# Performance work log

Measured on AMD Instinct MI355X. Metric: run time of the kernel, lower is better.

The kernel has to match this reference:

```python
import jax, jax.numpy as jnp
import numpy as np
from jax import lax

B, N, C = 8, 1024, 768
H, D = 12, 64
K = 3  # conv kernel size


def dwconv_over_batch(x, w, b):
    """Faithful port of SpatialDepthWisePerHeadConvolution as used in this module.
    x: [B, N, H, D]. The original code treats dim0 (B) as the conv length axis.
    w: [H*D, 1, K] depthwise kernel, b: [H*D].
    Returns [B, N, H, D].
    """
    b_, n_, h_, d_ = x.shape
    xc = jnp.transpose(x, (1, 2, 3, 0)).reshape(n_, h_ * d_, b_)  # [N, HD, B]
    y = lax.conv_general_dilated(
        xc, w, window_strides=(1,), padding=[(K - 1, K - 1)],
        feature_group_count=h_ * d_, dimension_numbers=("NCH", "OIH", "NCH"))
    y = y[:, :, :b_] + b[None, :, None]  # causal slice (drop last K-1)
    return jnp.transpose(y.reshape(n_, h_, d_, b_), (3, 0, 1, 2))


def setup_inputs() -> dict:
    key = jax.random.key(0)
    ks = jax.random.split(key, 12)
    s = 0.02
    inp = {
        "x": jax.random.normal(ks[0], (B, N, C), jnp.float32),
        "wq": jax.random.normal(ks[1], (C, H * D), jnp.float32) * s,
        "wk": jax.random.normal(ks[2], (C, H * D), jnp.float32) * s,
        "wv": jax.random.normal(ks[3], (C, H * D), jnp.float32) * s,
        "bv": jnp.zeros((H * D,), jnp.float32),
        "cq_w": jax.random.normal(ks[4], (H * D, 1, K), jnp.float32) * s,
        "cq_b": jnp.zeros((H * D,), jnp.float32),
        "ck_w": jax.random.normal(ks[5], (H * D, 1, K), jnp.float32) * s,
        "ck_b": jnp.zeros((H * D,), jnp.float32),
        "cv_w": jax.random.normal(ks[6], (H * D, 1, K), jnp.float32) * s,
        "cv_b": jnp.zeros((H * D,), jnp.float32),
        "wo": jax.random.normal(ks[7], (C, C), jnp.float32) * s,
        "bo": jnp.zeros((C,), jnp.float32),
    }
    return inp


def reference(x, wq, wk, wv, bv, cq_w, cq_b, ck_w, ck_b, cv_w, cv_b, wo, bo):
    scale = (C // H) ** -0.5
    # linear -> [B,N,H,D]
    q = (x @ wq).reshape(B, N, H, D)
    k = (x @ wk).reshape(B, N, H, D)
    v = ((x @ wv) + bv).reshape(B, N, H, D)
    # per-head depthwise causal conv (over batch axis, as in the original code)
    q = dwconv_over_batch(q, cq_w, cq_b)
    k = dwconv_over_batch(k, ck_w, ck_b)
    v = dwconv_over_batch(v, cv_w, cv_b)
    # [B,H,N,D]
    q = jnp.transpose(q, (0, 2, 1, 3))
    k = jnp.transpose(k, (0, 2, 1, 3))
    v = jnp.transpose(v, (0, 2, 1, 3))
    scores = jnp.einsum("bhnd,bhmd->bhnm", q, k) * scale
    attn = jax.nn.softmax(scores, axis=-1)
    out = jnp.einsum("bhnm,bhmd->bhnd", attn, v)
    out = jnp.transpose(out, (0, 2, 1, 3)).reshape(B, N, C)
    return out @ wo + bo
```

## Files before the change

### kernel.cpp

```cpp
#include <hip/hip_runtime.h>
#include <math.h>

static constexpr int B_ = 8, N_ = 1024, C_ = 768, H_ = 12, D_ = 64;

typedef __bf16 bf16_t;
typedef bf16_t bf16x8 __attribute__((ext_vector_type(8)));
typedef float f32x4 __attribute__((ext_vector_type(4)));

#define MFMA32(a, b, c) __builtin_amdgcn_mfma_f32_16x16x32_bf16((a), (b), (c), 0, 0, 0)

__device__ __forceinline__ unsigned short f2bf(float f) {
    unsigned u = __builtin_bit_cast(unsigned, f);
    u += 0x7FFFu + ((u >> 16) & 1u);
    return (unsigned short)(u >> 16);
}

__device__ __forceinline__ float bf2f(unsigned short u) {
    return __builtin_bit_cast(float, (unsigned)u << 16);
}

__device__ __forceinline__ void gload16(void* lds, const void* g) {
    __builtin_amdgcn_global_load_lds(
        (const __attribute__((address_space(1))) unsigned int*)g,
        (__attribute__((address_space(3))) unsigned int*)lds, 16, 0, 0);
}

__device__ __forceinline__ int swz(int row, int kslot) {
    return row * 128 + (((kslot ^ row) & 7) << 4);
}

__global__ __launch_bounds__(256)
void castx_kernel(const float* __restrict__ in, unsigned short* __restrict__ out)
{
    const int i = blockIdx.x * 256 + threadIdx.x;
    const float4 a = ((const float4*)in)[2 * i];
    const float4 b = ((const float4*)in)[2 * i + 1];
    uint4 o;
    o.x = f2bf(a.x) | ((unsigned)f2bf(a.y) << 16);
    o.y = f2bf(a.z) | ((unsigned)f2bf(a.w) << 16);
    o.z = f2bf(b.x) | ((unsigned)f2bf(b.y) << 16);
    o.w = f2bf(b.z) | ((unsigned)f2bf(b.w) << 16);
    ((uint4*)out)[i] = o;
}

__global__ __launch_bounds__(256)
void castwT4_kernel(const float* w0, const float* w1, const float* w2, const float* w3,
                    unsigned short* o0, unsigned short* o1,
                    unsigned short* o2, unsigned short* o3)
{
    const float* w; unsigned short* wT;
    switch (blockIdx.z) {
        case 0:  w = w0; wT = o0; break;
        case 1:  w = w1; wT = o1; break;
        case 2:  w = w2; wT = o2; break;
        default: w = w3; wT = o3; break;
    }
    __shared__ float T[64][65];
    const int t = threadIdx.x;
    const int k0 = blockIdx.x * 64, n0 = blockIdx.y * 64;
    const int r = t >> 2, c0 = (t & 3) * 16;
#pragma unroll
    for (int j4 = 0; j4 < 4; ++j4) {
        const float4 v = *(const float4*)(w + (size_t)(k0 + r) * 768 + n0 + c0 + j4 * 4);
        T[r][c0 + j4 * 4 + 0] = v.x; T[r][c0 + j4 * 4 + 1] = v.y;
        T[r][c0 + j4 * 4 + 2] = v.z; T[r][c0 + j4 * 4 + 3] = v.w;
    }
    __syncthreads();
    const int nn = t >> 2;
    unsigned short o[16];
#pragma unroll
    for (int j = 0; j < 16; ++j) o[j] = f2bf(T[c0 + j][nn]);
    uint4* dst = (uint4*)(wT + (size_t)(n0 + nn) * 768 + k0 + c0);
    dst[0] = *(uint4*)(o); dst[1] = *(uint4*)(o + 8);
}

template <typename OutT>
__device__ __forceinline__ void gemm_body(const unsigned short* __restrict__ A,
                                          const unsigned short* __restrict__ BT,
                                          const float* __restrict__ bias,
                                          OutT* __restrict__ Cmat,
                                          int Ncols, int Kdim, int row0, int col0)
{
    __shared__ char As[128 * 128];
    __shared__ char Bs[128 * 128];

    const int tid = threadIdx.x, lane = tid & 63, w = tid >> 6;
    const int wr = w >> 1, wc = w & 1;
    const int slot = lane & 7, rsub = lane >> 3;

    f32x4 acc[4][4] = {};

    for (int k0 = 0; k0 < Kdim; k0 += 64) {
#pragma unroll
        for (int c = 0; c < 4; ++c) {
            const int chunk = c * 4 + w;
            const int r = chunk * 8 + rsub;
            gload16(As + chunk * 1024, A + (size_t)(row0 + r) * Kdim + k0 + 8 * (slot ^ (r & 7)));
            gload16(Bs + chunk * 1024, BT + (size_t)(col0 + r) * Kdim + k0 + 8 * (slot ^ (r & 7)));
        }
        __syncthreads();

#pragma unroll
        for (int kk = 0; kk < 2; ++kk) {
            const int kslot = kk * 4 + (lane >> 4);
            bf16x8 af[4], bf[4];
#pragma unroll
            for (int mi = 0; mi < 4; ++mi)
                af[mi] = *(const bf16x8*)(As + swz(wr * 64 + mi * 16 + (lane & 15), kslot));
#pragma unroll
            for (int ni = 0; ni < 4; ++ni)
                bf[ni] = *(const bf16x8*)(Bs + swz(wc * 64 + ni * 16 + (lane & 15), kslot));
#pragma unroll
            for (int mi = 0; mi < 4; ++mi)
#pragma unroll
                for (int ni = 0; ni < 4; ++ni)
                    acc[mi][ni] = MFMA32(af[mi], bf[ni], acc[mi][ni]);
        }
        __syncthreads();
    }

#pragma unroll
    for (int mi = 0; mi < 4; ++mi) {
        const int row = row0 + wr * 64 + mi * 16 + ((lane >> 4) << 2);
#pragma unroll
        for (int ni = 0; ni < 4; ++ni) {
            const int col = col0 + wc * 64 + ni * 16 + (lane & 15);
            const float bv_ = bias ? bias[col] : 0.f;
#pragma unroll
            for (int r = 0; r < 4; ++r) {
                const float v = acc[mi][ni][r] + bv_;
                if constexpr (sizeof(OutT) == 2)
                    Cmat[(size_t)(row + r) * Ncols + col] = (OutT)f2bf(v);
                else
                    Cmat[(size_t)(row + r) * Ncols + col] = v;
            }
        }
    }
}

__global__ __launch_bounds__(256)
void gemm_qkv(const unsigned short* __restrict__ xb,
              const unsigned short* __restrict__ wqT, const unsigned short* __restrict__ wkT,
              const unsigned short* __restrict__ wvT, const float* __restrict__ bv,
              unsigned short* __restrict__ q_lin, unsigned short* __restrict__ k_lin,
              unsigned short* __restrict__ v_lin)
{
    const int by = blockIdx.y, sel = by / 6, colt = by % 6;
    const unsigned short* BT; unsigned short* dst; const float* bias = nullptr;
    if (sel == 0)      { BT = wqT; dst = q_lin; }
    else if (sel == 1) { BT = wkT; dst = k_lin; }
    else               { BT = wvT; dst = v_lin; bias = bv; }
    gemm_body<unsigned short>(xb, BT, bias, dst, C_, C_, blockIdx.x * 128, colt * 128);
}

__global__ __launch_bounds__(256)
void gemm_proj(const unsigned short* __restrict__ A, const unsigned short* __restrict__ BT,
               const float* __restrict__ bias, float* __restrict__ Cmat)
{
    gemm_body<float>(A, BT, bias, Cmat, C_, C_, blockIdx.x * 128, blockIdx.y * 128);
}

__global__ __launch_bounds__(256)
void dwconv_qk(const unsigned short* __restrict__ qlin, const unsigned short* __restrict__ klin,
               const float* __restrict__ cq_w, const float* __restrict__ cq_b,
               const float* __restrict__ ck_w, const float* __restrict__ ck_b,
               unsigned short* __restrict__ qc, unsigned short* __restrict__ kc)
{
    const unsigned short* lin; const float* w; const float* bias;
    unsigned short* out;
    if (blockIdx.y == 0) { lin = qlin; w = cq_w; bias = cq_b; out = qc; }
    else                 { lin = klin; w = ck_w; bias = ck_b; out = kc; }

    const int i = blockIdx.x * 256 + threadIdx.x;
    const int c8 = i % (C_ / 8);
    const int n  = (i / (C_ / 8)) % N_;
    const int b  = i / ((C_ / 8) * N_);
    const int c  = c8 * 8;

    const uint4 z4 = make_uint4(0, 0, 0, 0);
    const uint4 x0 = (b >= 2) ? *(const uint4*)(lin + ((size_t)(b - 2) * N_ + n) * C_ + c) : z4;
    const uint4 x1 = (b >= 1) ? *(const uint4*)(lin + ((size_t)(b - 1) * N_ + n) * C_ + c) : z4;
    const uint4 x2 = *(const uint4*)(lin + ((size_t)b * N_ + n) * C_ + c);
    const unsigned short* u0 = (const unsigned short*)&x0;
    const unsigned short* u1 = (const unsigned short*)&x1;
    const unsigned short* u2 = (const unsigned short*)&x2;

    unsigned short y[8];
#pragma unroll
    for (int j = 0; j < 8; ++j) {
        const float v = w[(c + j) * 3 + 0] * bf2f(u0[j]) +
                        w[(c + j) * 3 + 1] * bf2f(u1[j]) +
                        w[(c + j) * 3 + 2] * bf2f(u2[j]) + bias[c + j];
        y[j] = f2bf(v);
    }
    const int h = c8 >> 3, d0 = (c8 & 7) * 8;
    *(uint4*)(out + (((size_t)b * H_ + h) * N_ + n) * 64 + d0) = *(uint4*)y;
}

__global__ __launch_bounds__(256)
void conv_v_transpose(const unsigned short* __restrict__ vlin, const float* __restrict__ w,
                      const float* __restrict__ bias, unsigned short* __restrict__ vt)
{
    __shared__ unsigned short T[64][72];
    const int t = threadIdx.x;
    const int n0 = blockIdx.x * 64, bh = blockIdx.y;
    const int b = bh / H_, h = bh % H_;
    const int r = t >> 2, c0 = (t & 3) * 16;
    const int cbase = h * 64 + c0;

    float acc[16];
#pragma unroll
    for (int i = 0; i < 16; ++i) acc[i] = bias[cbase + i];
#pragma unroll
    for (int j = 0; j < 3; ++j) {
        const int bb = b - 2 + j;
        if (bb < 0) continue;
        const unsigned short* src = vlin + ((size_t)bb * N_ + n0 + r) * C_ + cbase;
        const uint4 va = *(const uint4*)src;
        const uint4 vb2 = *(const uint4*)(src + 8);
        const unsigned short* u = (const unsigned short*)&va;
        const unsigned short* u2 = (const unsigned short*)&vb2;
#pragma unroll
        for (int i = 0; i < 8; ++i)  acc[i]     += w[(cbase + i) * 3 + j] * bf2f(u[i]);
#pragma unroll
        for (int i = 0; i < 8; ++i)  acc[8 + i] += w[(cbase + 8 + i) * 3 + j] * bf2f(u2[i]);
    }
    unsigned short tmp[16];
#pragma unroll
    for (int i = 0; i < 16; ++i) tmp[i] = f2bf(acc[i]);
    *(uint4*)&T[r][c0] = *(uint4*)tmp;
    *(uint4*)&T[r][c0 + 8] = *(uint4*)(tmp + 8);
    __syncthreads();

    const int d = t >> 2;
    unsigned short o[16];
#pragma unroll
    for (int i = 0; i < 16; ++i) o[i] = T[c0 + i][d];
    uint4* dst = (uint4*)(vt + ((size_t)bh * 64 + d) * N_ + n0 + c0);
    dst[0] = *(uint4*)o; dst[1] = *(uint4*)(o + 8);
}

__global__ __launch_bounds__(256)
void attn_mfma(const unsigned short* __restrict__ Qg, const unsigned short* __restrict__ Kg,
               const unsigned short* __restrict__ Vtg, unsigned short* __restrict__ Og)
{
    __shared__ char Pb[16384];
    __shared__ char Kb[2][8192];
    __shared__ char Vb[2][8192];

    const int tid = threadIdx.x, lane = tid & 63, w = tid >> 6;
    const int slot = lane & 7, rsub = lane >> 3;

    const int id = blockIdx.x;
    const int bh = (id & 7) * 12 + ((id >> 3) % 12);
    const int q0 = (id / 96) * 128;
    const int b = bh / H_, h = bh % H_;

    const unsigned short* Qp = Qg + (size_t)bh * N_ * 64;
    const unsigned short* Kp = Kg + (size_t)bh * N_ * 64;
    const unsigned short* Vp = Vtg + (size_t)bh * 64 * N_;

#pragma unroll
    for (int c = 0; c < 4; ++c) {
        const int chunk = c * 4 + w;
        const int r = chunk * 8 + rsub;
        gload16(Pb + chunk * 1024, Qp + (size_t)(q0 + r) * 64 + 8 * (slot ^ (r & 7)));
    }
#pragma unroll
    for (int c = 0; c < 2; ++c) {
        const int chunk = c * 4 + w;
        const int r = chunk * 8 + rsub;
        gload16(Kb[0] + chunk * 1024, Kp + (size_t)r * 64 + 8 * (slot ^ (r & 7)));
        gload16(Vb[0] + chunk * 1024, Vp + (size_t)r * N_ + 8 * (slot ^ (r & 7)));
    }
    __syncthreads();

    bf16x8 qf[2][2];
#pragma unroll
    for (int mi = 0; mi < 2; ++mi)
#pragma unroll
        for (int kk = 0; kk < 2; ++kk)
            qf[mi][kk] = *(const bf16x8*)(Pb + swz(w * 32 + mi * 16 + (lane & 15), kk * 4 + (lane >> 4)));

    f32x4 o[2][4] = {};
    float mrow[2][4], lrow[2][4];
#pragma unroll
    for (int mi = 0; mi < 2; ++mi)
#pragma unroll
        for (int r = 0; r < 4; ++r) { mrow[mi][r] = -1e30f; lrow[mi][r] = 0.f; }

    int buf = 0;
    for (int kt = 0; kt < N_ / 64; ++kt) {
        if (kt < N_ / 64 - 1) {
            const int nb = buf ^ 1;
#pragma unroll
            for (int c = 0; c < 2; ++c) {
                const int chunk = c * 4 + w;
                const int r = chunk * 8 + rsub;
                gload16(Kb[nb] + chunk * 1024, Kp + (size_t)((kt + 1) * 64 + r) * 64 + 8 * (slot ^ (r & 7)));
                gload16(Vb[nb] + chunk * 1024, Vp + (size_t)r * N_ + (kt + 1) * 64 + 8 * (slot ^ (r & 7)));
            }
        }

        f32x4 s[2][4] = {};
#pragma unroll
        for (int kk = 0; kk < 2; ++kk) {
            const int kslot = kk * 4 + (lane >> 4);
            bf16x8 kf[4];
#pragma unroll
            for (int ni = 0; ni < 4; ++ni)
                kf[ni] = *(const bf16x8*)(Kb[buf] + swz(ni * 16 + (lane & 15), kslot));
#pragma unroll
            for (int mi = 0; mi < 2; ++mi)
#pragma unroll
                for (int ni = 0; ni < 4; ++ni)
                    s[mi][ni] = MFMA32(qf[mi][kk], kf[ni], s[mi][ni]);
        }

#pragma unroll
        for (int mi = 0; mi < 2; ++mi) {
            float pv[4][4];
#pragma unroll
            for (int r = 0; r < 4; ++r) {
                const float a0 = s[mi][0][r] * 0.125f, a1 = s[mi][1][r] * 0.125f;
                const float a2 = s[mi][2][r] * 0.125f, a3 = s[mi][3][r] * 0.125f;
                pv[r][0] = a0; pv[r][1] = a1; pv[r][2] = a2; pv[r][3] = a3;
                float m0 = fmaxf(fmaxf(a0, a1), fmaxf(a2, a3));
#pragma unroll
                for (int mk = 1; mk < 16; mk <<= 1) m0 = fmaxf(m0, __shfl_xor(m0, mk));
                const float mold = mrow[mi][r];
                const float mnew = fmaxf(mold, m0);
                const float f = __expf(mold - mnew);
                mrow[mi][r] = mnew;
                float ssum = 0.f;
#pragma unroll
                for (int ni = 0; ni < 4; ++ni) {
                    const float e = __expf(pv[r][ni] - mnew);
                    pv[r][ni] = e; ssum += e;
                }
#pragma unroll
                for (int mk = 1; mk < 16; mk <<= 1) ssum += __shfl_xor(ssum, mk);
                lrow[mi][r] = lrow[mi][r] * f + ssum;
#pragma unroll
                for (int nd = 0; nd < 4; ++nd) o[mi][nd][r] *= f;
            }
            const int prow_base = w * 32 + mi * 16 + ((lane >> 4) << 2);
#pragma unroll
            for (int r = 0; r < 4; ++r) {
                const int m = prow_base + r;
                const int rowoff = m * 128, sw = (m & 7) << 4;
#pragma unroll
                for (int ni = 0; ni < 4; ++ni) {
                    const int col = ni * 16 + (lane & 15);
                    *(unsigned short*)(Pb + rowoff + ((col * 2) ^ sw)) = f2bf(pv[r][ni]);
                }
            }
        }

#pragma unroll
        for (int kk = 0; kk < 2; ++kk) {
            const int kslot = kk * 4 + (lane >> 4);
            bf16x8 pa[2], vf[4];
#pragma unroll
            for (int mi = 0; mi < 2; ++mi)
                pa[mi] = *(const bf16x8*)(Pb + swz(w * 32 + mi * 16 + (lane & 15), kslot));
#pragma unroll
            for (int nd = 0; nd < 4; ++nd)
                vf[nd] = *(const bf16x8*)(Vb[buf] + swz(nd * 16 + (lane & 15), kslot));
#pragma unroll
            for (int mi = 0; mi < 2; ++mi)
#pragma unroll
                for (int nd = 0; nd < 4; ++nd)
                    o[mi][nd] = MFMA32(pa[mi], vf[nd], o[mi][nd]);
        }

        __syncthreads();
        buf ^= 1;
    }

#pragma unroll
    for (int mi = 0; mi < 2; ++mi)
#pragma unroll
        for (int r = 0; r < 4; ++r) {
            const float inv = 1.0f / lrow[mi][r];
            const int qrow = q0 + w * 32 + mi * 16 + ((lane >> 4) << 2) + r;
            unsigned short* orow = Og + ((size_t)b * N_ + qrow) * C_ + h * D_ + (lane & 15);
#pragma unroll
            for (int nd = 0; nd < 4; ++nd) orow[nd * 16] = f2bf(o[mi][nd][r] * inv);
        }
}

extern "C" void kernel_launch(void* const* d_in, const int* in_sizes, int n_in,
                              void* d_out, int out_size, void* d_ws, size_t ws_size,
                              hipStream_t stream)
{
    (void)in_sizes; (void)n_in; (void)out_size; (void)ws_size;
    const float* x    = (const float*)d_in[0];
    const float* wq   = (const float*)d_in[1];
    const float* wk   = (const float*)d_in[2];
    const float* wv   = (const float*)d_in[3];
    const float* bv   = (const float*)d_in[4];
    const float* cq_w = (const float*)d_in[5];
    const float* cq_b = (const float*)d_in[6];
    const float* ck_w = (const float*)d_in[7];
    const float* ck_b = (const float*)d_in[8];
    const float* cv_w = (const float*)d_in[9];
    const float* cv_b = (const float*)d_in[10];
    const float* wo   = (const float*)d_in[11];
    const float* bo   = (const float*)d_in[12];
    float* out = (float*)d_out;

    char* wsb = (char*)d_ws;
    const size_t T  = (size_t)B_ * N_ * C_;
    const size_t WB = (size_t)2 * 589824;
    unsigned short* xb  = (unsigned short*)wsb;
    unsigned short* wqT = (unsigned short*)(wsb + 2 * T);
    unsigned short* wkT = wqT + 589824;
    unsigned short* wvT = wkT + 589824;
    unsigned short* woT = wvT + 589824;
    char* p = wsb + 2 * T + 4 * WB;
    unsigned short* q_lin = (unsigned short*)p;          p += 2 * T;
    unsigned short* k_lin = (unsigned short*)p;          p += 2 * T;
    unsigned short* v_lin = (unsigned short*)p;          p += 2 * T;
    unsigned short* qc    = (unsigned short*)p;          p += 2 * T;
    unsigned short* kc    = (unsigned short*)p;          p += 2 * T;
    unsigned short* vt    = (unsigned short*)p;          p += 2 * T;
    unsigned short* attn_out = xb;

    const int M = B_ * N_;

    castx_kernel<<<dim3((int)(T / 8 / 256)), 256, 0, stream>>>(x, xb);
    castwT4_kernel<<<dim3(12, 12, 4), 256, 0, stream>>>(wq, wk, wv, wo, wqT, wkT, wvT, woT);

    gemm_qkv<<<dim3(M / 128, 18), 256, 0, stream>>>(xb, wqT, wkT, wvT, bv, q_lin, k_lin, v_lin);

    dwconv_qk<<<dim3((int)(T / 8 / 256), 2), 256, 0, stream>>>(
        q_lin, k_lin, cq_w, cq_b, ck_w, ck_b, qc, kc);
    conv_v_transpose<<<dim3(N_ / 64, B_ * H_), 256, 0, stream>>>(v_lin, cv_w, cv_b, vt);

    attn_mfma<<<dim3(768), 256, 0, stream>>>(qc, kc, vt, attn_out);

    gemm_proj<<<dim3(M / 128, C_ / 128), 256, 0, stream>>>(attn_out, woT, bo, out);
}
```

Baseline: 308.3 us.

## Keep softmax probabilities in registers via transposed S and lazy max rescale

The attention kernel now computes S transposed (K as the A operand), so each lane holds a full column of scores for one query row. This lets the bf16 probabilities feed the PV MFMA (16x16x16) directly from registers, removing the LDS round-trip through the P buffer and its staging of Q, which is now loaded straight from global memory. Softmax uses exp2 with a prescaled log2e factor and rescales the running max only when it grows by more than 8, which cuts exp and shuffle work per row. In exchange, PV uses the smaller MFMA shape, and the output is written with packed 8-byte stores.

Measured after the change: 277.8 us. -9.9%, faster.

```diff
diff --git a/kernel.cpp b/kernel.cpp
--- a/kernel.cpp
+++ b/kernel.cpp
@@ -5,9 +5,13 @@
 
 typedef __bf16 bf16_t;
 typedef bf16_t bf16x8 __attribute__((ext_vector_type(8)));
+typedef bf16_t bf16x4 __attribute__((ext_vector_type(4)));
+typedef short short4v __attribute__((ext_vector_type(4)));
 typedef float f32x4 __attribute__((ext_vector_type(4)));
 
 #define MFMA32(a, b, c) __builtin_amdgcn_mfma_f32_16x16x32_bf16((a), (b), (c), 0, 0, 0)
+#define MFMA16(a, b, c) __builtin_amdgcn_mfma_f32_16x16x16bf16_1k( \
+    __builtin_bit_cast(short4v, (a)), __builtin_bit_cast(short4v, (b)), (c), 0, 0, 0)
 
 __device__ __forceinline__ unsigned short f2bf(float f) {
     unsigned u = __builtin_bit_cast(unsigned, f);
@@ -244,11 +248,11 @@
 void attn_mfma(const unsigned short* __restrict__ Qg, const unsigned short* __restrict__ Kg,
                const unsigned short* __restrict__ Vtg, unsigned short* __restrict__ Og)
 {
-    __shared__ char Pb[16384];
     __shared__ char Kb[2][8192];
     __shared__ char Vb[2][8192];
 
     const int tid = threadIdx.x, lane = tid & 63, w = tid >> 6;
+    const int g = lane >> 4, q = lane & 15;
     const int slot = lane & 7, rsub = lane >> 3;
 
     const int id = blockIdx.x;
@@ -260,34 +264,24 @@
     const unsigned short* Kp = Kg + (size_t)bh * N_ * 64;
     const unsigned short* Vp = Vtg + (size_t)bh * 64 * N_;
 
-#pragma unroll
-    for (int c = 0; c < 4; ++c) {
-        const int chunk = c * 4 + w;
-        const int r = chunk * 8 + rsub;
-        gload16(Pb + chunk * 1024, Qp + (size_t)(q0 + r) * 64 + 8 * (slot ^ (r & 7)));
-    }
+    bf16x8 qf[2][2];
+#pragma unroll
+    for (int mi = 0; mi < 2; ++mi)
+#pragma unroll
+        for (int kk = 0; kk < 2; ++kk)
+            qf[mi][kk] = *(const bf16x8*)(Qp + (size_t)(q0 + w * 32 + mi * 16 + q) * 64 + kk * 32 + g * 8);
+
 #pragma unroll
     for (int c = 0; c < 2; ++c) {
-        const int chunk = c * 4 + w;
-        const int r = chunk * 8 + rsub;
+        const int chunk = c * 4 + w, r = chunk * 8 + rsub;
         gload16(Kb[0] + chunk * 1024, Kp + (size_t)r * 64 + 8 * (slot ^ (r & 7)));
         gload16(Vb[0] + chunk * 1024, Vp + (size_t)r * N_ + 8 * (slot ^ (r & 7)));
     }
     __syncthreads();
 
-    bf16x8 qf[2][2];
-#pragma unroll
-    for (int mi = 0; mi < 2; ++mi)
-#pragma unroll
-        for (int kk = 0; kk < 2; ++kk)
-            qf[mi][kk] = *(const bf16x8*)(Pb + swz(w * 32 + mi * 16 + (lane & 15), kk * 4 + (lane >> 4)));
-
     f32x4 o[2][4] = {};
-    float mrow[2][4], lrow[2][4];
-#pragma unroll
-    for (int mi = 0; mi < 2; ++mi)
-#pragma unroll
-        for (int r = 0; r < 4; ++r) { mrow[mi][r] = -1e30f; lrow[mi][r] = 0.f; }
+    float mrun[2] = {0.f, 0.f}, lrun[2] = {0.f, 0.f};
+    const float cs = 0.18033688011112042f;
 
     int buf = 0;
     for (int kt = 0; kt < N_ / 64; ++kt) {
@@ -295,8 +289,7 @@
             const int nb = buf ^ 1;
 #pragma unroll
             for (int c = 0; c < 2; ++c) {
-                const int chunk = c * 4 + w;
-                const int r = chunk * 8 + rsub;
+                const int chunk = c * 4 + w, r = chunk * 8 + rsub;
                 gload16(Kb[nb] + chunk * 1024, Kp + (size_t)((kt + 1) * 64 + r) * 64 + 8 * (slot ^ (r & 7)));
                 gload16(Vb[nb] + chunk * 1024, Vp + (size_t)r * N_ + (kt + 1) * 64 + 8 * (slot ^ (r & 7)));
             }
@@ -305,73 +298,72 @@
         f32x4 s[2][4] = {};
 #pragma unroll
         for (int kk = 0; kk < 2; ++kk) {
-            const int kslot = kk * 4 + (lane >> 4);
+            const int kslot = kk * 4 + g;
             bf16x8 kf[4];
 #pragma unroll
             for (int ni = 0; ni < 4; ++ni)
-                kf[ni] = *(const bf16x8*)(Kb[buf] + swz(ni * 16 + (lane & 15), kslot));
+                kf[ni] = *(const bf16x8*)(Kb[buf] + swz(ni * 16 + q, kslot));
 #pragma unroll
             for (int mi = 0; mi < 2; ++mi)
 #pragma unroll
                 for (int ni = 0; ni < 4; ++ni)
-                    s[mi][ni] = MFMA32(qf[mi][kk], kf[ni], s[mi][ni]);
-        }
-
+                    s[mi][ni] = MFMA32(kf[ni], qf[mi][kk], s[mi][ni]);
+        }
+
+        bf16x4 pf[2][4];
 #pragma unroll
         for (int mi = 0; mi < 2; ++mi) {
-            float pv[4][4];
-#pragma unroll
-            for (int r = 0; r < 4; ++r) {
-                const float a0 = s[mi][0][r] * 0.125f, a1 = s[mi][1][r] * 0.125f;
-                const float a2 = s[mi][2][r] * 0.125f, a3 = s[mi][3][r] * 0.125f;
-                pv[r][0] = a0; pv[r][1] = a1; pv[r][2] = a2; pv[r][3] = a3;
-                float m0 = fmaxf(fmaxf(a0, a1), fmaxf(a2, a3));
-#pragma unroll
-                for (int mk = 1; mk < 16; mk <<= 1) m0 = fmaxf(m0, __shfl_xor(m0, mk));
-                const float mold = mrow[mi][r];
-                const float mnew = fmaxf(mold, m0);
-                const float f = __expf(mold - mnew);
-                mrow[mi][r] = mnew;
-                float ssum = 0.f;
-#pragma unroll
-                for (int ni = 0; ni < 4; ++ni) {
-                    const float e = __expf(pv[r][ni] - mnew);
-                    pv[r][ni] = e; ssum += e;
-                }
-#pragma unroll
-                for (int mk = 1; mk < 16; mk <<= 1) ssum += __shfl_xor(ssum, mk);
-                lrow[mi][r] = lrow[mi][r] * f + ssum;
-#pragma unroll
-                for (int nd = 0; nd < 4; ++nd) o[mi][nd][r] *= f;
+            float t[4][4];
+#pragma unroll
+            for (int ni = 0; ni < 4; ++ni)
+#pragma unroll
+                for (int rg = 0; rg < 4; ++rg) t[ni][rg] = s[mi][ni][rg] * cs;
+            float m0 = t[0][0];
+#pragma unroll
+            for (int ni = 0; ni < 4; ++ni)
+#pragma unroll
+                for (int rg = 0; rg < 4; ++rg) m0 = fmaxf(m0, t[ni][rg]);
+            m0 = fmaxf(m0, __shfl_xor(m0, 16));
+            m0 = fmaxf(m0, __shfl_xor(m0, 32));
+            if (__any(m0 > mrun[mi] + 8.f)) {
+                const float mnew = fmaxf(mrun[mi], m0);
+                const float f = exp2f(mrun[mi] - mnew);
+                lrun[mi] *= f;
+#pragma unroll
+                for (int nd = 0; nd < 4; ++nd) o[mi][nd] *= f;
+                mrun[mi] = mnew;
             }
-            const int prow_base = w * 32 + mi * 16 + ((lane >> 4) << 2);
-#pragma unroll
-            for (int r = 0; r < 4; ++r) {
-                const int m = prow_base + r;
-                const int rowoff = m * 128, sw = (m & 7) << 4;
-#pragma unroll
-                for (int ni = 0; ni < 4; ++ni) {
-                    const int col = ni * 16 + (lane & 15);
-                    *(unsigned short*)(Pb + rowoff + ((col * 2) ^ sw)) = f2bf(pv[r][ni]);
-                }
+            float sum = 0.f;
+#pragma unroll
+            for (int ni = 0; ni < 4; ++ni) {
+                const float p0 = exp2f(t[ni][0] - mrun[mi]);
+                const float p1 = exp2f(t[ni][1] - mrun[mi]);
+                const float p2 = exp2f(t[ni][2] - mrun[mi]);
+                const float p3 = exp2f(t[ni][3] - mrun[mi]);
+                sum += (p0 + p1) + (p2 + p3);
+                bf16x4 pk;
+                pk[0] = (bf16_t)p0; pk[1] = (bf16_t)p1; pk[2] = (bf16_t)p2; pk[3] = (bf16_t)p3;
+                pf[mi][ni] = pk;
             }
-        }
-
-#pragma unroll
-        for (int kk = 0; kk < 2; ++kk) {
-            const int kslot = kk * 4 + (lane >> 4);
-            bf16x8 pa[2], vf[4];
+            sum += __shfl_xor(sum, 16);
+            sum += __shfl_xor(sum, 32);
+            lrun[mi] += sum;
+        }
+
+#pragma unroll
+        for (int ni = 0; ni < 4; ++ni) {
+            bf16x4 vf[4];
+#pragma unroll
+            for (int nd = 0; nd < 4; ++nd) {
+                const int d = nd * 16 + q;
+                vf[nd] = *(const bf16x4*)(Vb[buf] + d * 128 +
+                          ((((2 * ni + (g >> 1)) ^ (d & 7))) << 4) + 8 * (g & 1));
+            }
 #pragma unroll
             for (int mi = 0; mi < 2; ++mi)
-                pa[mi] = *(const bf16x8*)(Pb + swz(w * 32 + mi * 16 + (lane & 15), kslot));
-#pragma unroll
-            for (int nd = 0; nd < 4; ++nd)
-                vf[nd] = *(const bf16x8*)(Vb[buf] + swz(nd * 16 + (lane & 15), kslot));
-#pragma unroll
-            for (int mi = 0; mi < 2; ++mi)
 #pragma unroll
                 for (int nd = 0; nd < 4; ++nd)
-                    o[mi][nd] = MFMA32(pa[mi], vf[nd], o[mi][nd]);
+                    o[mi][nd] = MFMA16(vf[nd], pf[mi][ni], o[mi][nd]);
         }
 
         __syncthreads();
@@ -379,15 +371,18 @@
     }
 
 #pragma unroll
-    for (int mi = 0; mi < 2; ++mi)
-#pragma unroll
-        for (int r = 0; r < 4; ++r) {
-            const float inv = 1.0f / lrow[mi][r];
-            const int qrow = q0 + w * 32 + mi * 16 + ((lane >> 4) << 2) + r;
-            unsigned short* orow = Og + ((size_t)b * N_ + qrow) * C_ + h * D_ + (lane & 15);
-#pragma unroll
-            for (int nd = 0; nd < 4; ++nd) orow[nd * 16] = f2bf(o[mi][nd][r] * inv);
-        }
+    for (int mi = 0; mi < 2; ++mi) {
+        const float inv = 1.0f / lrun[mi];
+        const int qrow = q0 + w * 32 + mi * 16 + q;
+        unsigned short* orow = Og + ((size_t)b * N_ + qrow) * C_ + h * D_;
+#pragma unroll
+        for (int nd = 0; nd < 4; ++nd) {
+            unsigned short pk[4];
+#pragma unroll
+            for (int rg = 0; rg < 4; ++rg) pk[rg] = f2bf(o[mi][nd][rg] * inv);
+            *(uint2*)(orow + nd * 16 + 4 * g) = *(uint2*)pk;
+        }
+    }
 }
 
 extern "C" void kernel_launch(void* const* d_in, const int* in_sizes, int n_in,
```
